# Kernel optimization log

Measured on AMD Instinct MI355X. Metric: run time of the kernel, lower is better.

The kernel has to match this reference:

```python
import jax, jax.numpy as jnp
import numpy as np

B = 8          # batch
HID = 1024     # hidden_size
NH = 8         # query heads
KVH = 1        # kv heads (GQA)
HD = 256       # head_dim
NL = 18        # layers
MLP = 4096     # intermediate size
AH = 50        # action_horizon (suffix len)
AD = 32        # action_dim
P = 1037       # prefix_len
EPS = 1e-6
ROPE_BASE = 10000.0
SCALE = HD ** -0.5
NEG = -2.3819763e38


def _rms(x):
    return x * jax.lax.rsqrt(jnp.mean(x * x, axis=-1, keepdims=True) + EPS)


def _ada_norm(x, cond, W):
    # AdaRMS: cond -> (scale, shift, gate); normed*(1+scale)+shift, gate returned for gated residual
    scale, shift, gate = jnp.split(cond @ W, 3, axis=-1)
    return _rms(x) * (1.0 + scale[:, None, :]) + shift[:, None, :], gate[:, None, :]


def _rope(x, pos):
    # x: [B, heads, S, HD], pos: [B, S]; HF rotate-half convention
    inv = 1.0 / (ROPE_BASE ** (jnp.arange(0, HD, 2, dtype=jnp.float32) / HD))
    freqs = pos[:, :, None].astype(jnp.float32) * inv          # [B,S,HD/2]
    cos = jnp.tile(jnp.cos(freqs), (1, 1, 2))[:, None]          # [B,1,S,HD]
    sin = jnp.tile(jnp.sin(freqs), (1, 1, 2))[:, None]
    x1, x2 = jnp.split(x, 2, axis=-1)
    return x * cos + jnp.concatenate([-x2, x1], axis=-1) * sin


def setup_inputs() -> dict:
    key = jax.random.key(0)
    ks = jax.random.split(key, 24)
    s = 0.02
    return {
        'prefix_keys': jax.random.normal(ks[0], (B, NL, KVH, P, HD), jnp.float32),
        'prefix_values': jax.random.normal(ks[1], (B, NL, KVH, P, HD), jnp.float32),
        'prefix_pad_masks': jnp.ones((B, P), dtype=bool),
        'x_t': jax.random.normal(ks[2], (B, AH, AD), jnp.float32),
        'timestep': jax.random.uniform(ks[3], (B,), jnp.float32),
        'Wq': jax.random.normal(ks[4], (NL, HID, NH * HD), jnp.float32) * s,
        'Wk': jax.random.normal(ks[5], (NL, HID, KVH * HD), jnp.float32) * s,
        'Wv': jax.random.normal(ks[6], (NL, HID, KVH * HD), jnp.float32) * s,
        'Wo': jax.random.normal(ks[7], (NL, NH * HD, HID), jnp.float32) * s,
        'Wg': jax.random.normal(ks[8], (NL, HID, MLP), jnp.float32) * s,
        'Wu': jax.random.normal(ks[9], (NL, HID, MLP), jnp.float32) * s,
        'Wd': jax.random.normal(ks[10], (NL, MLP, HID), jnp.float32) * s,
        'A1': jax.random.normal(ks[11], (NL, HID, 3 * HID), jnp.float32) * s,
        'A2': jax.random.normal(ks[12], (NL, HID, 3 * HID), jnp.float32) * s,
        'Af': jax.random.normal(ks[13], (HID, 3 * HID), jnp.float32) * s,
        'W_act_in': jax.random.normal(ks[14], (AD, HID), jnp.float32) * s,
        'b_act_in': jnp.zeros((HID,), jnp.float32),
        'W_act_out': jax.random.normal(ks[15], (HID, AD), jnp.float32) * s,
        'b_act_out': jnp.zeros((AD,), jnp.float32),
        'W_t_in': jax.random.normal(ks[16], (HID, HID), jnp.float32) * s,
        'b_t_in': jnp.zeros((HID,), jnp.float32),
        'W_t_out': jax.random.normal(ks[17], (HID, HID), jnp.float32) * s,
        'b_t_out': jnp.zeros((HID,), jnp.float32),
    }


def reference(prefix_keys, prefix_values, prefix_pad_masks, x_t, timestep,
              Wq, Wk, Wv, Wo, Wg, Wu, Wd, A1, A2, Af,
              W_act_in, b_act_in, W_act_out, b_act_out,
              W_t_in, b_t_in, W_t_out, b_t_out):
    b = x_t.shape[0]
    # --- time embedding (sinusoidal over log-spaced periods) -> AdaRMS cond ---
    frac = jnp.linspace(0.0, 1.0, HID // 2)
    period = 0.004 * (4.0 / 0.004) ** frac
    sin_in = (2.0 * jnp.pi / period)[None, :] * timestep[:, None]
    temb = jnp.concatenate([jnp.sin(sin_in), jnp.cos(sin_in)], axis=1)  # [B,HID]
    cond = jax.nn.silu(jax.nn.silu(temb @ W_t_in + b_t_in) @ W_t_out + b_t_out)

    # --- action input projection ---
    h = x_t @ W_act_in + b_act_in  # [B,AH,HID]

    # --- attention mask & positions ---
    # suffix att_masks = [1,0,...,0] -> cumsum constant -> suffix block fully visible
    suf_att = jnp.ones((b, AH, AH), dtype=bool)
    s2p = jnp.broadcast_to(prefix_pad_masks[:, None, :], (b, AH, P))
    full = jnp.concatenate([s2p, suf_att], axis=2)          # [B,AH,P+AH]
    bias = jnp.where(full, 0.0, NEG).astype(jnp.float32)[:, None]  # [B,1,AH,P+AH]
    offs = jnp.sum(prefix_pad_masks.astype(jnp.int32), axis=-1, keepdims=True)
    pos = offs + jnp.arange(AH)                              # [B,AH]

    def layer(hcur, p):
        wq, wk, wv, wo, wg, wu, wd, a1, a2, ck, cv = p
        normed, gate = _ada_norm(hcur, cond, a1)
        q = (normed @ wq).reshape(b, AH, NH, HD).transpose(0, 2, 1, 3)
        k = (normed @ wk).reshape(b, AH, KVH, HD).transpose(0, 2, 1, 3)
        v = (normed @ wv).reshape(b, AH, KVH, HD).transpose(0, 2, 1, 3)
        q = _rope(q, pos)
        k = _rope(k, pos)
        fk = jnp.concatenate([ck, k], axis=2)   # [B,KVH,P+AH,HD]
        fv = jnp.concatenate([cv, v], axis=2)
        rep = NH // KVH
        fk = jnp.repeat(fk, rep, axis=1)
        fv = jnp.repeat(fv, rep, axis=1)
        scores = jnp.einsum('bhqd,bhkd->bhqk', q, fk) * SCALE + bias
        attn = jax.nn.softmax(scores, axis=-1)
        o = jnp.einsum('bhqk,bhkd->bhqd', attn, fv)
        o = o.transpose(0, 2, 1, 3).reshape(b, AH, NH * HD) @ wo
        h1 = hcur + gate * o                     # gated residual 1
        n2, gate2 = _ada_norm(h1, cond, a2)
        mlp = (jax.nn.gelu(n2 @ wg, approximate=True) * (n2 @ wu)) @ wd
        return h1 + gate2 * mlp, None            # gated residual 2

    pk = jnp.moveaxis(prefix_keys, 1, 0)   # [NL,B,KVH,P,HD]
    pv = jnp.moveaxis(prefix_values, 1, 0)
    h, _ = jax.lax.scan(layer, h, (Wq, Wk, Wv, Wo, Wg, Wu, Wd, A1, A2, pk, pv))

    out, _ = _ada_norm(h, cond, Af)
    return out @ W_act_out + b_act_out  # [B,AH,AD]
```

## Files before the change

### kernel.cpp

```cpp
#include <hip/hip_runtime.h>

typedef unsigned short u16;
typedef unsigned int   u32;
typedef __attribute__((ext_vector_type(8))) short bh8;
typedef __attribute__((ext_vector_type(4))) float f4;

constexpr int BATCH = 8, HIDN = 1024, NHEAD = 8, HD = 256, NLAY = 18, DMLP = 4096;
constexpr int AHOR = 50, ADIMN = 32, PFXN = 1037, SEQN = 1087, NSTR = 17, MR = 400, MP = 512;
constexpr float EPSV = 1e-6f, NEGV = -2.3819763e38f, QSCALE = 0.0625f;
constexpr size_t ADASL = (size_t)37 * 3 * BATCH * HIDN;
constexpr int SW64 = 90, SW32 = 138, SKT = 266, SPT = 74, SVT = 90;

static __device__ __forceinline__ u16 f2bf(float x){
  union{float f; u32 u;} v; v.f = x;
  u32 r = (v.u + 0x7FFFu + ((v.u >> 16) & 1u)) >> 16;
  return (u16)r;
}
static __device__ __forceinline__ float bf2f(u16 u){
  union{u32 u; float f;} v; v.u = ((u32)u) << 16; return v.f;
}
static __device__ __forceinline__ u32 pack2(float a, float b){
  return (u32)f2bf(a) | ((u32)f2bf(b) << 16);
}
static __device__ __forceinline__ f4 MFMA(bh8 a, bh8 b, f4 c){
  return __builtin_amdgcn_mfma_f32_16x16x32_bf16(a, b, c, 0, 0, 0);
}
static __device__ __forceinline__ float siluf_(float x){ return x / (1.f + __expf(-x)); }
static __device__ __forceinline__ float geluf_(float x){
  float y = 0.7978845608028654f * (x + 0.044715f * x * x * x);
  float e = __expf(2.f * y);
  return 0.5f * x * (2.f - 2.f / (e + 1.f));
}

__global__ void k_prep(const int* __restrict__ mask, const float* __restrict__ ts,
                       float* __restrict__ temb, int* __restrict__ offs,
                       float* __restrict__ ropec, float* __restrict__ ropes)
{
  int t = threadIdx.x;
  {
    int b = t >> 5, l = t & 31;
    const int* mp = mask + b * PFXN;
    int s = 0;
    for (int k = l; k < PFXN; k += 32) s += (mp[k] != 0);
    #pragma unroll
    for (int off = 16; off >= 1; off >>= 1) s += __shfl_xor(s, off);
    if (l == 0) offs[b] = s;
  }
  for (int i = t; i < BATCH * 512; i += 256){
    int b = i >> 9, j = i & 511;
    float frac = (float)j * (1.0f / 511.0f);
    float period = 0.004f * __expf(frac * 6.907755278982137f);
    float arg = (6.283185307179586f / period) * ts[b];
    float s, c; sincosf(arg, &s, &c);
    temb[b * HIDN + j] = s;
    temb[b * HIDN + 512 + j] = c;
  }
  __syncthreads();
  for (int i = t; i < BATCH * AHOR * 128; i += 256){
    int d = i & 127, bt = i >> 7, b = bt / AHOR, tt = bt % AHOR;
    float inv = __expf(-((float)d * (1.f / 128.f)) * 9.210340371976184f);
    float arg = (float)(offs[b] + tt) * inv;
    float s, c; sincosf(arg, &s, &c);
    ropec[i] = c; ropes[i] = s;
  }
}

__global__ void k_tproj(const float* __restrict__ X, const float* __restrict__ W,
                        const float* __restrict__ bias, float* __restrict__ out)
{
  __shared__ float xs[BATCH * HIDN];
  __shared__ float red[BATCH][8][32];
  int t = threadIdx.x;
  for (int i = t; i < BATCH * HIDN; i += 256) xs[i] = X[i];
  __syncthreads();
  int c = t & 31, kp = t >> 5;
  int c0 = blockIdx.x * 32;
  float acc[BATCH];
  #pragma unroll
  for (int b = 0; b < BATCH; ++b) acc[b] = 0.f;
  for (int k = kp * 128; k < kp * 128 + 128; ++k){
    float w = W[(size_t)k * HIDN + c0 + c];
    #pragma unroll
    for (int b = 0; b < BATCH; ++b) acc[b] += xs[b * HIDN + k] * w;
  }
  #pragma unroll
  for (int b = 0; b < BATCH; ++b) red[b][kp][c] = acc[b];
  __syncthreads();
  int b2 = t >> 5, c2 = t & 31;
  float s = bias[c0 + c2];
  #pragma unroll
  for (int kp2 = 0; kp2 < 8; ++kp2) s += red[b2][kp2][c2];
  out[b2 * HIDN + c0 + c2] = siluf_(s);
}

__global__ void k_ada_part(const float* __restrict__ cond, const float* __restrict__ A1,
                           const float* __restrict__ A2, const float* __restrict__ Af,
                           float* __restrict__ adap)
{
  __shared__ float cs[BATCH * 128];
  int t = threadIdx.x;
  int y = blockIdx.y, ks = blockIdx.z;
  int k0 = ks * 128;
  for (int i = t; i < BATCH * 128; i += 256){
    int b = i >> 7, kk = i & 127;
    cs[i] = cond[b * HIDN + k0 + kk];
  }
  __syncthreads();
  const float* A = (y < NLAY) ? (A1 + (size_t)y * HIDN * 3072)
                  : (y < 2 * NLAY) ? (A2 + (size_t)(y - NLAY) * HIDN * 3072) : Af;
  int n = (blockIdx.x * 256 + t) * 4;
  f4 acc[BATCH];
  #pragma unroll
  for (int b = 0; b < BATCH; ++b) acc[b] = (f4){0.f,0.f,0.f,0.f};
  const float* ap = A + (size_t)k0 * 3072 + n;
  for (int kk = 0; kk < 128; kk += 8){
    f4 av[8];
    #pragma unroll
    for (int j = 0; j < 8; ++j) av[j] = *(const f4*)(ap + (size_t)(kk + j) * 3072);
    #pragma unroll
    for (int j = 0; j < 8; ++j){
      #pragma unroll
      for (int b = 0; b < BATCH; ++b) acc[b] += av[j] * cs[b * 128 + kk + j];
    }
  }
  int comp = n >> 10, nn = n & 1023;
  float* o = adap + (size_t)ks * ADASL + ((size_t)y * 3 + comp) * BATCH * HIDN + nn;
  #pragma unroll
  for (int b = 0; b < BATCH; ++b) *(f4*)(o + b * HIDN) = acc[b];
}

__global__ void k_ada_red(const float* __restrict__ adap, float* __restrict__ ada)
{
  size_t i = ((size_t)blockIdx.x * 256 + threadIdx.x) * 8;
  f4 a0 = {0,0,0,0}, a1 = {0,0,0,0};
  #pragma unroll
  for (int ks = 0; ks < 8; ++ks){
    const float* p = adap + (size_t)ks * ADASL + i;
    a0 += *(const f4*)p;
    a1 += *(const f4*)(p + 4);
  }
  *(f4*)(ada + i) = a0;
  *(f4*)(ada + i + 4) = a1;
}

__global__ void k_hin(const float* __restrict__ xt, const float* __restrict__ W,
                      const float* __restrict__ bias, float* __restrict__ h)
{
  int r = blockIdx.x;
  int t = threadIdx.x; int c0 = t * 4;
  __shared__ float xs[ADIMN];
  if (t < ADIMN) xs[t] = xt[r * ADIMN + t];
  __syncthreads();
  float a0 = bias[c0], a1 = bias[c0+1], a2 = bias[c0+2], a3 = bias[c0+3];
  for (int k = 0; k < ADIMN; ++k){
    float x = xs[k];
    const float* wp = W + k * HIDN + c0;
    a0 += x * wp[0]; a1 += x * wp[1]; a2 += x * wp[2]; a3 += x * wp[3];
  }
  float* hp = h + (size_t)r * HIDN + c0;
  hp[0] = a0; hp[1] = a1; hp[2] = a2; hp[3] = a3;
}

__global__ void k_resnorm(int mode, int np,
    const float* __restrict__ base, const u16* __restrict__ parts,
    const float* __restrict__ gate, const float* __restrict__ sc,
    const float* __restrict__ sh, float* __restrict__ outres,
    u16* __restrict__ fragA)
{
  __shared__ float redl[4];
  int t = threadIdx.x;
  int c = t * 4;
  for (int i = 0; i < 2; ++i){
    int r = blockIdx.x * 2 + i;
    bool live = (r < MR);
    float4 v = {0.f,0.f,0.f,0.f};
    int b = live ? (r / AHOR) : 0;
    if (live){
      v = *(const float4*)(base + (size_t)r * HIDN + c);
      if (mode){
        float s0 = 0, s1 = 0, s2 = 0, s3 = 0;
        #pragma unroll 4
        for (int p = 0; p < np; ++p){
          ushort4 u4 = *(const ushort4*)(parts + ((size_t)p * MP + r) * HIDN + c);
          s0 += bf2f(u4.x); s1 += bf2f(u4.y); s2 += bf2f(u4.z); s3 += bf2f(u4.w);
        }
        float4 gp = *(const float4*)(gate + b * HIDN + c);
        v.x += gp.x * s0; v.y += gp.y * s1; v.z += gp.z * s2; v.w += gp.w * s3;
        *(float4*)(outres + (size_t)r * HIDN + c) = v;
      }
    }
    float ss = v.x*v.x + v.y*v.y + v.z*v.z + v.w*v.w;
    #pragma unroll
    for (int off = 1; off < 64; off <<= 1) ss += __shfl_xor(ss, off);
    if ((t & 63) == 0) redl[t >> 6] = ss;
    __syncthreads();
    float tot = redl[0] + redl[1] + redl[2] + redl[3];
    __syncthreads();
    u16* dst = fragA + ((size_t)(c >> 3)) * MP * 8 + (size_t)r * 8 + (c & 7);
    ushort4 ov;
    if (live){
      float rstd = rsqrtf(tot * (1.0f / HIDN) + EPSV);
      const float4 scp = *(const float4*)(sc + b * HIDN + c);
      const float4 shp = *(const float4*)(sh + b * HIDN + c);
      ov.x = f2bf(v.x * rstd * (1.f + scp.x) + shp.x);
      ov.y = f2bf(v.y * rstd * (1.f + scp.y) + shp.y);
      ov.z = f2bf(v.z * rstd * (1.f + scp.z) + shp.z);
      ov.w = f2bf(v.w * rstd * (1.f + scp.w) + shp.w);
    } else {
      ov.x = ov.y = ov.z = ov.w = 0;
    }
    *(ushort4*)dst = ov;
  }
}

template<int NOUTER>
static __device__ __forceinline__ void gemm_core32w(
    const u16* __restrict__ fa,
    const float* __restrict__ Wa, int cb0,
    const float* __restrict__ Wb, int cb1,
    int wN, u16* lds, f4 acc[4][2])
{
  const int tid = threadIdx.x;
  const int lane = tid & 63, wave = tid >> 6;
  const int l15 = lane & 15, g = lane >> 4;
  const int wrow = wave * 64;
  const int c4 = (tid & 7) * 4;
  const int r0 = (tid >> 3) * 2;
  const float* wcol = (c4 < 16) ? (Wa + cb0 + c4) : (Wb + cb1 + (c4 - 16));
  f4 preA[3], preB[3];
  preA[0] = *(const f4*)(wcol + (size_t)r0 * wN);
  preB[0] = *(const f4*)(wcol + (size_t)(r0 + 1) * wN);
  if (NOUTER > 1){
    preA[1] = *(const f4*)(wcol + (size_t)(128 + r0) * wN);
    preB[1] = *(const f4*)(wcol + (size_t)(129 + r0) * wN);
  }
  if (NOUTER > 2){
    preA[2] = *(const f4*)(wcol + (size_t)(256 + r0) * wN);
    preB[2] = *(const f4*)(wcol + (size_t)(257 + r0) * wN);
  }
  #pragma unroll
  for (int i = 0; i < 4; ++i)
    *(u32*)(lds + (c4 + i) * SW32 + r0) = pack2(preA[0][i], preB[0][i]);
  __syncthreads();
  #pragma unroll
  for (int ko = 0; ko < NOUTER; ++ko){
    u16* ldsr = lds + (ko & 1) * (32 * SW32);
    bh8 a01[2][4], a23[2][4];
    #pragma unroll
    for (int kk = 0; kk < 2; ++kk){
      const u16* ap = fa + ((size_t)(ko * 16 + kk * 4 + g) * MP + wrow + l15) * 8;
      #pragma unroll
      for (int mf = 0; mf < 4; ++mf) a01[kk][mf] = *(const bh8*)(ap + mf * 128);
    }
    if (ko + 3 < NOUTER){
      preA[ko % 3] = *(const f4*)(wcol + (size_t)((ko + 3) * 128 + r0) * wN);
      preB[ko % 3] = *(const f4*)(wcol + (size_t)((ko + 3) * 128 + r0 + 1) * wN);
    }
    #pragma unroll
    for (int kk = 2; kk < 4; ++kk){
      const u16* ap = fa + ((size_t)(ko * 16 + kk * 4 + g) * MP + wrow + l15) * 8;
      #pragma unroll
      for (int mf = 0; mf < 4; ++mf) a23[kk - 2][mf] = *(const bh8*)(ap + mf * 128);
    }
    #pragma unroll
    for (int kk = 0; kk < 2; ++kk){
      bh8 bb[2];
      #pragma unroll
      for (int nf = 0; nf < 2; ++nf) bb[nf] = *(const bh8*)(ldsr + (nf * 16 + l15) * SW32 + kk * 32 + g * 8);
      #pragma unroll
      for (int mf = 0; mf < 4; ++mf){
        acc[mf][0] = MFMA(a01[kk][mf], bb[0], acc[mf][0]);
        acc[mf][1] = MFMA(a01[kk][mf], bb[1], acc[mf][1]);
      }
    }
    #pragma unroll
    for (int kk = 2; kk < 4; ++kk){
      bh8 bb[2];
      #pragma unroll
      for (int nf = 0; nf < 2; ++nf) bb[nf] = *(const bh8*)(ldsr + (nf * 16 + l15) * SW32 + kk * 32 + g * 8);
      #pragma unroll
      for (int mf = 0; mf < 4; ++mf){
        acc[mf][0] = MFMA(a23[kk - 2][mf], bb[0], acc[mf][0]);
        acc[mf][1] = MFMA(a23[kk - 2][mf], bb[1], acc[mf][1]);
      }
    }
    if (ko + 1 < NOUTER){
      u16* ldsw = lds + ((ko + 1) & 1) * (32 * SW32);
      const int sl = (ko + 1) % 3;
      #pragma unroll
      for (int i = 0; i < 4; ++i)
        *(u32*)(ldsw + (c4 + i) * SW32 + r0) = pack2(preA[sl][i], preB[sl][i]);
      __syncthreads();
    }
  }
}

__global__ __launch_bounds__(512) void k_qkvrope(
    const u16* __restrict__ n1, const float* __restrict__ Wq,
    const float* __restrict__ Wk, const float* __restrict__ Wv,
    const float* __restrict__ ropec, const float* __restrict__ ropes,
    u16* __restrict__ qf, u16* __restrict__ ks, u16* __restrict__ vs)
{
  __shared__ u16 lds[2 * 32 * SW32];
  int bx = blockIdx.x;
  const float *Wa, *Wb; int cb0, cb1, wN, type, head = 0, fb = 0, d0 = 0;
  if (bx < 64){ type = 0; head = bx >> 3; fb = (bx & 7) * 16; Wa = Wq; Wb = Wq; wN = NHEAD * HD; cb0 = head * HD + fb; cb1 = cb0 + 128; }
  else if (bx < 72){ type = 1; fb = (bx - 64) * 16; Wa = Wk; Wb = Wk; wN = HD; cb0 = fb; cb1 = fb + 128; }
  else { type = 2; d0 = (bx - 72) * 32; Wa = Wv; Wb = Wv; wN = HD; cb0 = d0; cb1 = d0 + 16; }
  f4 acc[4][2];
  #pragma unroll
  for (int i = 0; i < 4; ++i)
    #pragma unroll
    for (int j = 0; j < 2; ++j) acc[i][j] = (f4){0.f, 0.f, 0.f, 0.f};
  gemm_core32w<8>(n1, Wa, cb0, Wb, cb1, wN, lds, acc);
  int tid = threadIdx.x, lane = tid & 63, wave = tid >> 6, l15 = lane & 15, g = lane >> 4;
  int wrow = wave * 64;
  #pragma unroll
  for (int mf = 0; mf < 4; ++mf)
    #pragma unroll
    for (int r = 0; r < 4; ++r){
      int row = wrow + mf * 16 + 4 * g + r;
      if (row >= MR) continue;
      int b = row / AHOR, tt = row - b * AHOR;
      float lo = acc[mf][0][r], hi = acc[mf][1][r];
      if (type == 2){
        size_t vb = ((size_t)(b * AHOR + tt)) * HD;
        vs[vb + d0 + l15] = f2bf(lo);
        vs[vb + d0 + 16 + l15] = f2bf(hi);
      } else {
        int dA = fb + l15;
        float cz = ropec[(size_t)(b * AHOR + tt) * 128 + dA];
        float sz = ropes[(size_t)(b * AHOR + tt) * 128 + dA];
        float oA = lo * cz - hi * sz;
        float oB = hi * cz + lo * sz;
        if (type == 0){
          oA *= QSCALE; oB *= QSCALE;
          int rowp = head * AHOR + tt;
          int dB = dA + 128;
          qf[((size_t)(b * 32 + (dA >> 3))) * MP * 8 + (size_t)rowp * 8 + (dA & 7)] = f2bf(oA);
          qf[((size_t)(b * 32 + (dB >> 3))) * MP * 8 + (size_t)rowp * 8 + (dB & 7)] = f2bf(oB);
        } else {
          size_t kb = ((size_t)(b * AHOR + tt)) * HD;
          ks[kb + dA] = f2bf(oA);
          ks[kb + dA + 128] = f2bf(oB);
        }
      }
    }
}

__global__ __launch_bounds__(512) void k_attn(
    const u16* __restrict__ qf, const u16* __restrict__ kss, const u16* __restrict__ vss,
    const float* __restrict__ pk, const float* __restrict__ pv,
    const int* __restrict__ mask, int layer,
    u16* __restrict__ opart, float* __restrict__ mrow, float* __restrict__ lrow)
{
  __shared__ u16 kv[256 * SVT];
  __shared__ u16 plds[256 * SPT];
  int s = blockIdx.x, b = blockIdx.y, z = blockIdx.z;
  int tid = threadIdx.x, lane = tid & 63, wave = tid >> 6, l15 = lane & 15, g = lane >> 4;
  int zb = z * 256;
  int wbase = wave * 32;
  {
    int key = tid >> 3, dblk = (tid & 7) * 32;
    int kg = s * 64 + key;
    u32* dst = (u32*)(kv + key * SKT + dblk);
    if (kg < PFXN){
      const float4* src = (const float4*)(pk + (((size_t)b * NLAY + layer) * PFXN + kg) * HD + dblk);
      #pragma unroll
      for (int j = 0; j < 8; ++j){ float4 v = src[j]; dst[2*j] = pack2(v.x, v.y); dst[2*j+1] = pack2(v.z, v.w); }
    } else if (kg < SEQN){
      const u32* src = (const u32*)(kss + ((size_t)b * AHOR + (kg - PFXN)) * HD + dblk);
      #pragma unroll
      for (int j = 0; j < 16; ++j) dst[j] = src[j];
    } else {
      #pragma unroll
      for (int j = 0; j < 16; ++j) dst[j] = 0;
    }
  }
  float vreg[32];
  int vkey = tid >> 3, vdb = (tid & 7) * 32;
  {
    int kgv = s * 64 + vkey;
    if (kgv < PFXN){
      const float4* src = (const float4*)(pv + (((size_t)b * NLAY + layer) * PFXN + kgv) * HD + vdb);
      #pragma unroll
      for (int j = 0; j < 8; ++j){ float4 v = src[j]; vreg[4*j] = v.x; vreg[4*j+1] = v.y; vreg[4*j+2] = v.z; vreg[4*j+3] = v.w; }
    } else if (kgv < SEQN){
      const u32* src = (const u32*)(vss + ((size_t)b * AHOR + (kgv - PFXN)) * HD + vdb);
      #pragma unroll
      for (int j = 0; j < 16; ++j){ u32 u = src[j]; vreg[2*j] = bf2f((u16)(u & 0xFFFF)); vreg[2*j+1] = bf2f((u16)(u >> 16)); }
    } else {
      #pragma unroll
      for (int j = 0; j < 32; ++j) vreg[j] = 0.f;
    }
  }
  bool valid[4];
  #pragma unroll
  for (int nf = 0; nf < 4; ++nf){
    int kgc = s * 64 + nf * 16 + l15;
    valid[nf] = (kgc < PFXN) ? (mask[b * PFXN + kgc] != 0) : (kgc < SEQN);
  }
  __syncthreads();
  f4 acc[2][4];
  #pragma unroll
  for (int i = 0; i < 2; ++i)
    #pragma unroll
    for (int j = 0; j < 4; ++j) acc[i][j] = (f4){0.f,0.f,0.f,0.f};
  const u16* qb = qf + (size_t)b * 32 * MP * 8;
  #pragma unroll
  for (int ko = 0; ko < 4; ++ko)
    #pragma unroll
    for (int kk = 0; kk < 2; ++kk){
      int kc = ko * 8 + kk * 4 + g;
      bh8 a[2], bb[4];
      const u16* ap = qb + ((size_t)kc * MP + zb + wbase + l15) * 8;
      #pragma unroll
      for (int mf = 0; mf < 2; ++mf) a[mf] = *(const bh8*)(ap + mf * 128);
      #pragma unroll
      for (int nf = 0; nf < 4; ++nf) bb[nf] = *(const bh8*)(kv + (nf * 16 + l15) * SKT + ko * 64 + kk * 32 + g * 8);
      #pragma unroll
      for (int mf = 0; mf < 2; ++mf)
        #pragma unroll
        for (int nf = 0; nf < 4; ++nf) acc[mf][nf] = MFMA(a[mf], bb[nf], acc[mf][nf]);
    }
  #pragma unroll
  for (int nf = 0; nf < 4; ++nf) if (!valid[nf]){
    #pragma unroll
    for (int mf = 0; mf < 2; ++mf){
      acc[mf][nf][0] = NEGV; acc[mf][nf][1] = NEGV; acc[mf][nf][2] = NEGV; acc[mf][nf][3] = NEGV;
    }
  }
  #pragma unroll
  for (int mf = 0; mf < 2; ++mf)
    #pragma unroll
    for (int r = 0; r < 4; ++r){
      float m0 = fmaxf(fmaxf(acc[mf][0][r], acc[mf][1][r]), fmaxf(acc[mf][2][r], acc[mf][3][r]));
      #pragma unroll
      for (int off = 1; off < 16; off <<= 1) m0 = fmaxf(m0, __shfl_xor(m0, off));
      int lr = wbase + mf * 16 + 4 * g + r;
      float sum = 0.f;
      #pragma unroll
      for (int nf = 0; nf < 4; ++nf){
        float p = __expf(acc[mf][nf][r] - m0);
        sum += p;
        plds[lr * SPT + nf * 16 + l15] = f2bf(p);
      }
      #pragma unroll
      for (int off = 1; off < 16; off <<= 1) sum += __shfl_xor(sum, off);
      if (l15 == 0){
        mrow[((size_t)b * NSTR + s) * MP + zb + lr] = m0;
        lrow[((size_t)b * NSTR + s) * MP + zb + lr] = sum;
      }
    }
  __syncthreads();
  {
    #pragma unroll
    for (int j = 0; j < 32; ++j){
      int dloc = vdb + j;
      kv[dloc * SVT + ((dloc >> 5) & 3) * 8 + vkey] = f2bf(vreg[j]);
    }
  }
  __syncthreads();
  #pragma unroll
  for (int dc = 0; dc < 4; ++dc){
    f4 oc[2][4];
    #pragma unroll
    for (int i = 0; i < 2; ++i)
      #pragma unroll
      for (int j = 0; j < 4; ++j) oc[i][j] = (f4){0.f,0.f,0.f,0.f};
    #pragma unroll
    for (int kk = 0; kk < 2; ++kk){
      bh8 a[2], bb[4];
      #pragma unroll
      for (int mf = 0; mf < 2; ++mf) a[mf] = *(const bh8*)(plds + (wbase + mf * 16 + l15) * SPT + kk * 32 + g * 8);
      #pragma unroll
      for (int nf = 0; nf < 4; ++nf){
        int dcol = dc * 64 + nf * 16 + l15;
        bb[nf] = *(const bh8*)(kv + dcol * SVT + ((dcol >> 5) & 3) * 8 + kk * 32 + g * 8);
      }
      #pragma unroll
      for (int mf = 0; mf < 2; ++mf)
        #pragma unroll
        for (int nf = 0; nf < 4; ++nf) oc[mf][nf] = MFMA(a[mf], bb[nf], oc[mf][nf]);
    }
    #pragma unroll
    for (int mf = 0; mf < 2; ++mf)
      #pragma unroll
      for (int r = 0; r < 4; ++r){
        int row = zb + wbase + mf * 16 + 4 * g + r;
        if (row < MR){
          #pragma unroll
          for (int nf = 0; nf < 4; ++nf){
            int d = dc * 64 + nf * 16 + l15;
            opart[(((size_t)b * NSTR + s) * MR + row) * HD + d] = f2bf(oc[mf][nf][r]);
          }
        }
      }
  }
}

__global__ void k_comb(const u16* __restrict__ opart, const float* __restrict__ mrow,
                       const float* __restrict__ lrow, u16* __restrict__ ao)
{
  int b = blockIdx.y;
  int t = threadIdx.x;
  int d4 = (t & 63) * 4;
  int row = blockIdx.x * 4 + (t >> 6);
  float M = -3.0e38f;
  for (int s2 = 0; s2 < NSTR; ++s2) M = fmaxf(M, mrow[((size_t)b * NSTR + s2) * MP + row]);
  float L = 0.f;
  float o0 = 0.f, o1 = 0.f, o2 = 0.f, o3 = 0.f;
  for (int s2 = 0; s2 < NSTR; ++s2){
    float w = __expf(mrow[((size_t)b * NSTR + s2) * MP + row] - M);
    L += w * lrow[((size_t)b * NSTR + s2) * MP + row];
    ushort4 u4 = *(const ushort4*)(opart + (((size_t)b * NSTR + s2) * MR + row) * HD + d4);
    o0 += w * bf2f(u4.x); o1 += w * bf2f(u4.y); o2 += w * bf2f(u4.z); o3 += w * bf2f(u4.w);
  }
  float rL = 1.0f / L;
  int h = row / AHOR, tt = row - h * AHOR;
  int col = h * HD + d4;
  int rg = b * AHOR + tt;
  ushort4 ov;
  ov.x = f2bf(o0 * rL); ov.y = f2bf(o1 * rL); ov.z = f2bf(o2 * rL); ov.w = f2bf(o3 * rL);
  *(ushort4*)(ao + ((size_t)(col >> 3)) * MP * 8 + (size_t)rg * 8 + (col & 7)) = ov;
}

template<int NOUTER>
__global__ __launch_bounds__(512) void k_gemm_part32(
    const u16* __restrict__ fa, const float* __restrict__ W, int wN,
    u16* __restrict__ outp)
{
  __shared__ u16 lds[2 * 32 * SW32];
  int n0 = blockIdx.x * 32;
  int ksl = blockIdx.y;
  const u16* fa_s = fa + (size_t)(ksl * NOUTER * 16) * MP * 8;
  const float* W_s = W + (size_t)(ksl * NOUTER * 128) * wN;
  f4 acc[4][2];
  #pragma unroll
  for (int i = 0; i < 4; ++i)
    #pragma unroll
    for (int j = 0; j < 2; ++j) acc[i][j] = (f4){0.f,0.f,0.f,0.f};
  gemm_core32w<NOUTER>(fa_s, W_s, n0, W_s, n0 + 16, wN, lds, acc);
  int tid = threadIdx.x, lane = tid & 63, wave = tid >> 6, l15 = lane & 15, g = lane >> 4;
  int wrow = wave * 64;
  #pragma unroll
  for (int mf = 0; mf < 4; ++mf)
    #pragma unroll
    for (int r = 0; r < 4; ++r){
      int row = wrow + mf * 16 + 4 * g + r;
      outp[((size_t)ksl * MP + row) * 1024 + n0 + l15] = f2bf(acc[mf][0][r]);
      outp[((size_t)ksl * MP + row) * 1024 + n0 + 16 + l15] = f2bf(acc[mf][1][r]);
    }
}

__global__ __launch_bounds__(512) void k_mlpup(
    const u16* __restrict__ n2, const float* __restrict__ Wg, const float* __restrict__ Wu,
    u16* __restrict__ mlpf)
{
  __shared__ u16 lds[2 * 32 * SW32];
  int n0 = blockIdx.x * 16;
  f4 acc[4][2];
  #pragma unroll
  for (int i = 0; i < 4; ++i)
    #pragma unroll
    for (int j = 0; j < 2; ++j) acc[i][j] = (f4){0.f,0.f,0.f,0.f};
  gemm_core32w<8>(n2, Wg, n0, Wu, n0, DMLP, lds, acc);
  int tid = threadIdx.x, lane = tid & 63, wave = tid >> 6, l15 = lane & 15, g = lane >> 4;
  int wrow = wave * 64;
  #pragma unroll
  for (int mf = 0; mf < 4; ++mf)
    #pragma unroll
    for (int r = 0; r < 4; ++r){
      int row = wrow + mf * 16 + 4 * g + r;
      int col = n0 + l15;
      float gg = acc[mf][0][r], uu = acc[mf][1][r];
      float act = geluf_(gg) * uu;
      mlpf[((size_t)(col >> 3)) * MP * 8 + (size_t)row * 8 + (col & 7)] = f2bf(act);
    }
}

__global__ void k_out(const u16* __restrict__ nfr, const float* __restrict__ W,
                      const float* __restrict__ bias, float* __restrict__ out)
{
  int t = threadIdx.x;
  int row = blockIdx.x * 8 + (t >> 5);
  int c = t & 31;
  float acc = bias[c];
  for (int kc = 0; kc < 128; ++kc){
    bh8 v = *(const bh8*)(nfr + ((size_t)kc * MP + row) * 8);
    #pragma unroll
    for (int j = 0; j < 8; ++j)
      acc += bf2f((u16)v[j]) * W[(kc * 8 + j) * ADIMN + c];
  }
  out[row * ADIMN + c] = acc;
}

extern "C" void kernel_launch(void* const* d_in, const int* in_sizes, int n_in,
                              void* d_out, int out_size, void* d_ws, size_t ws_size,
                              hipStream_t stream)
{
  const float* pk  = (const float*)d_in[0];
  const float* pv  = (const float*)d_in[1];
  const int*   msk = (const int*)d_in[2];
  const float* xt  = (const float*)d_in[3];
  const float* ts  = (const float*)d_in[4];
  const float* Wq  = (const float*)d_in[5];
  const float* Wk  = (const float*)d_in[6];
  const float* Wv  = (const float*)d_in[7];
  const float* Wo  = (const float*)d_in[8];
  const float* Wg  = (const float*)d_in[9];
  const float* Wu  = (const float*)d_in[10];
  const float* Wd  = (const float*)d_in[11];
  const float* A1  = (const float*)d_in[12];
  const float* A2  = (const float*)d_in[13];
  const float* Af  = (const float*)d_in[14];
  const float* Wai = (const float*)d_in[15];
  const float* bai = (const float*)d_in[16];
  const float* Wao = (const float*)d_in[17];
  const float* bao = (const float*)d_in[18];
  const float* Wti = (const float*)d_in[19];
  const float* bti = (const float*)d_in[20];
  const float* Wto = (const float*)d_in[21];
  const float* bto = (const float*)d_in[22];

  char* w = (char*)d_ws;
  size_t off = 0;
  auto alloc = [&](size_t bytes) -> char* {
    char* p = w + off; off += (bytes + 255) & ~(size_t)255; return p;
  };
  float* temb  = (float*)alloc((size_t)BATCH * HIDN * 4);
  float* ttmp  = (float*)alloc((size_t)BATCH * HIDN * 4);
  float* cond  = (float*)alloc((size_t)BATCH * HIDN * 4);
  int*   offs  = (int*)alloc(BATCH * 4);
  float* ropec = (float*)alloc((size_t)BATCH * AHOR * 128 * 4);
  float* ropes = (float*)alloc((size_t)BATCH * AHOR * 128 * 4);
  float* ada   = (float*)alloc(ADASL * 4);
  float* adap  = (float*)alloc(8 * ADASL * 4);
  float* h     = (float*)alloc((size_t)MR * HIDN * 4);
  float* h1    = (float*)alloc((size_t)MR * HIDN * 4);
  u16*   n1    = (u16*)alloc((size_t)128 * MP * 8 * 2);
  u16*   n2    = (u16*)alloc((size_t)128 * MP * 8 * 2);
  u16*   qf    = (u16*)alloc((size_t)BATCH * 32 * MP * 8 * 2);
  u16*   kss   = (u16*)alloc((size_t)BATCH * AHOR * HD * 2);
  u16*   vss   = (u16*)alloc((size_t)BATCH * AHOR * HD * 2);
  u16*   opart = (u16*)alloc((size_t)BATCH * NSTR * MR * HD * 2);
  float* mrow  = (float*)alloc((size_t)BATCH * NSTR * MP * 4);
  float* lrow  = (float*)alloc((size_t)BATCH * NSTR * MP * 4);
  u16*   ao    = (u16*)alloc((size_t)256 * MP * 8 * 2);
  u16*   opp   = (u16*)alloc((size_t)8 * MP * 1024 * 2);
  u16*   mlpf  = (u16*)alloc((size_t)512 * MP * 8 * 2);
  u16*   mdp   = (u16*)alloc((size_t)8 * MP * 1024 * 2);
  if (off > ws_size) return;

  k_prep<<<1, 256, 0, stream>>>(msk, ts, temb, offs, ropec, ropes);
  k_tproj<<<32, 256, 0, stream>>>(temb, Wti, bti, ttmp);
  k_tproj<<<32, 256, 0, stream>>>(ttmp, Wto, bto, cond);
  k_ada_part<<<dim3(3, 37, 8), 256, 0, stream>>>(cond, A1, A2, Af, adap);
  k_ada_red<<<444, 256, 0, stream>>>(adap, ada);
  k_hin<<<MR, 256, 0, stream>>>(xt, Wai, bai, h);

  auto AP = [&](int y, int comp){ return ada + ((size_t)y * 3 + comp) * BATCH * HIDN; };

  k_resnorm<<<256, 256, 0, stream>>>(0, 0, h, nullptr, nullptr, AP(0,0), AP(0,1), nullptr, n1);

  for (int l = 0; l < NLAY; ++l){
    k_qkvrope<<<80, 512, 0, stream>>>(n1, Wq + (size_t)l * HIDN * NHEAD * HD,
                                      Wk + (size_t)l * HIDN * HD, Wv + (size_t)l * HIDN * HD,
                                      ropec, ropes, qf, kss, vss);
    k_attn<<<dim3(NSTR, BATCH, 2), 512, 0, stream>>>(qf, kss, vss, pk, pv, msk, l, opart, mrow, lrow);
    k_comb<<<dim3(100, BATCH), 256, 0, stream>>>(opart, mrow, lrow, ao);
    k_gemm_part32<2><<<dim3(32, 8), 512, 0, stream>>>(ao, Wo + (size_t)l * 2048 * 1024, 1024, opp);
    k_resnorm<<<256, 256, 0, stream>>>(1, 8, h, opp, AP(l,2), AP(NLAY+l,0), AP(NLAY+l,1), h1, n2);
    k_mlpup<<<256, 512, 0, stream>>>(n2, Wg + (size_t)l * HIDN * DMLP, Wu + (size_t)l * HIDN * DMLP, mlpf);
    k_gemm_part32<4><<<dim3(32, 8), 512, 0, stream>>>(mlpf, Wd + (size_t)l * DMLP * 1024, 1024, mdp);
    const float* nsc = (l < NLAY - 1) ? AP(l + 1, 0) : AP(36, 0);
    const float* nsh = (l < NLAY - 1) ? AP(l + 1, 1) : AP(36, 1);
    k_resnorm<<<256, 256, 0, stream>>>(2, 8, h1, mdp, AP(NLAY+l,2), nsc, nsh, h, n1);
  }
  k_out<<<50, 256, 0, stream>>>(n1, Wao, bao, (float*)d_out);
}
```

Measured before the change: 2.832 ms.

## Process two key tiles per attention block with online softmax, halving split count

```diff
diff --git a/kernel.cpp b/kernel.cpp
--- a/kernel.cpp
+++ b/kernel.cpp
@@ -6,10 +6,11 @@
 typedef __attribute__((ext_vector_type(4))) float f4;
 
 constexpr int BATCH = 8, HIDN = 1024, NHEAD = 8, HD = 256, NLAY = 18, DMLP = 4096;
-constexpr int AHOR = 50, ADIMN = 32, PFXN = 1037, SEQN = 1087, NSTR = 17, MR = 400, MP = 512;
+constexpr int AHOR = 50, ADIMN = 32, PFXN = 1037, SEQN = 1087, MR = 400, MP = 512;
+constexpr int NGRP = 9;
 constexpr float EPSV = 1e-6f, NEGV = -2.3819763e38f, QSCALE = 0.0625f;
 constexpr size_t ADASL = (size_t)37 * 3 * BATCH * HIDN;
-constexpr int SW64 = 90, SW32 = 138, SKT = 266, SPT = 74, SVT = 90;
+constexpr int SW32 = 138, SKT = 266, SPT = 74, SVT = 90;
 
 static __device__ __forceinline__ u16 f2bf(float x){
   union{float f; u32 u;} v; v.f = x;
@@ -360,129 +361,159 @@
   int tid = threadIdx.x, lane = tid & 63, wave = tid >> 6, l15 = lane & 15, g = lane >> 4;
   int zb = z * 256;
   int wbase = wave * 32;
-  {
-    int key = tid >> 3, dblk = (tid & 7) * 32;
-    int kg = s * 64 + key;
-    u32* dst = (u32*)(kv + key * SKT + dblk);
-    if (kg < PFXN){
-      const float4* src = (const float4*)(pk + (((size_t)b * NLAY + layer) * PFXN + kg) * HD + dblk);
-      #pragma unroll
-      for (int j = 0; j < 8; ++j){ float4 v = src[j]; dst[2*j] = pack2(v.x, v.y); dst[2*j+1] = pack2(v.z, v.w); }
-    } else if (kg < SEQN){
-      const u32* src = (const u32*)(kss + ((size_t)b * AHOR + (kg - PFXN)) * HD + dblk);
-      #pragma unroll
-      for (int j = 0; j < 16; ++j) dst[j] = src[j];
-    } else {
-      #pragma unroll
-      for (int j = 0; j < 16; ++j) dst[j] = 0;
-    }
-  }
-  float vreg[32];
-  int vkey = tid >> 3, vdb = (tid & 7) * 32;
-  {
-    int kgv = s * 64 + vkey;
-    if (kgv < PFXN){
-      const float4* src = (const float4*)(pv + (((size_t)b * NLAY + layer) * PFXN + kgv) * HD + vdb);
-      #pragma unroll
-      for (int j = 0; j < 8; ++j){ float4 v = src[j]; vreg[4*j] = v.x; vreg[4*j+1] = v.y; vreg[4*j+2] = v.z; vreg[4*j+3] = v.w; }
-    } else if (kgv < SEQN){
-      const u32* src = (const u32*)(vss + ((size_t)b * AHOR + (kgv - PFXN)) * HD + vdb);
-      #pragma unroll
-      for (int j = 0; j < 16; ++j){ u32 u = src[j]; vreg[2*j] = bf2f((u16)(u & 0xFFFF)); vreg[2*j+1] = bf2f((u16)(u >> 16)); }
-    } else {
-      #pragma unroll
-      for (int j = 0; j < 32; ++j) vreg[j] = 0.f;
-    }
-  }
-  bool valid[4];
-  #pragma unroll
-  for (int nf = 0; nf < 4; ++nf){
-    int kgc = s * 64 + nf * 16 + l15;
-    valid[nf] = (kgc < PFXN) ? (mask[b * PFXN + kgc] != 0) : (kgc < SEQN);
-  }
-  __syncthreads();
-  f4 acc[2][4];
-  #pragma unroll
-  for (int i = 0; i < 2; ++i)
-    #pragma unroll
-    for (int j = 0; j < 4; ++j) acc[i][j] = (f4){0.f,0.f,0.f,0.f};
-  const u16* qb = qf + (size_t)b * 32 * MP * 8;
-  #pragma unroll
-  for (int ko = 0; ko < 4; ++ko)
-    #pragma unroll
-    for (int kk = 0; kk < 2; ++kk){
-      int kc = ko * 8 + kk * 4 + g;
-      bh8 a[2], bb[4];
-      const u16* ap = qb + ((size_t)kc * MP + zb + wbase + l15) * 8;
-      #pragma unroll
-      for (int mf = 0; mf < 2; ++mf) a[mf] = *(const bh8*)(ap + mf * 128);
-      #pragma unroll
-      for (int nf = 0; nf < 4; ++nf) bb[nf] = *(const bh8*)(kv + (nf * 16 + l15) * SKT + ko * 64 + kk * 32 + g * 8);
-      #pragma unroll
-      for (int mf = 0; mf < 2; ++mf)
-        #pragma unroll
-        for (int nf = 0; nf < 4; ++nf) acc[mf][nf] = MFMA(a[mf], bb[nf], acc[mf][nf]);
-    }
-  #pragma unroll
-  for (int nf = 0; nf < 4; ++nf) if (!valid[nf]){
-    #pragma unroll
-    for (int mf = 0; mf < 2; ++mf){
-      acc[mf][nf][0] = NEGV; acc[mf][nf][1] = NEGV; acc[mf][nf][2] = NEGV; acc[mf][nf][3] = NEGV;
-    }
-  }
+  f4 oc[4][2][4];
+  #pragma unroll
+  for (int dc = 0; dc < 4; ++dc)
+    #pragma unroll
+    for (int mf = 0; mf < 2; ++mf)
+      #pragma unroll
+      for (int nf = 0; nf < 4; ++nf) oc[dc][mf][nf] = (f4){0.f,0.f,0.f,0.f};
+  float mrun[2][4], lrun[2][4];
   #pragma unroll
   for (int mf = 0; mf < 2; ++mf)
     #pragma unroll
+    for (int r = 0; r < 4; ++r){ mrun[mf][r] = -3.0e38f; lrun[mf][r] = 0.f; }
+
+  #pragma unroll
+  for (int kt = 0; kt < 2; ++kt){
+    int kbase = s * 128 + kt * 64;
+    {
+      int key = tid >> 3, dblk = (tid & 7) * 32;
+      int kg = kbase + key;
+      u32* dst = (u32*)(kv + key * SKT + dblk);
+      if (kg < PFXN){
+        const float4* src = (const float4*)(pk + (((size_t)b * NLAY + layer) * PFXN + kg) * HD + dblk);
+        #pragma unroll
+        for (int j = 0; j < 8; ++j){ float4 v = src[j]; dst[2*j] = pack2(v.x, v.y); dst[2*j+1] = pack2(v.z, v.w); }
+      } else if (kg < SEQN){
+        const u32* src = (const u32*)(kss + ((size_t)b * AHOR + (kg - PFXN)) * HD + dblk);
+        #pragma unroll
+        for (int j = 0; j < 16; ++j) dst[j] = src[j];
+      } else {
+        #pragma unroll
+        for (int j = 0; j < 16; ++j) dst[j] = 0;
+      }
+    }
+    float vreg[32];
+    int vkey = tid >> 3, vdb = (tid & 7) * 32;
+    {
+      int kgv = kbase + vkey;
+      if (kgv < PFXN){
+        const float4* src = (const float4*)(pv + (((size_t)b * NLAY + layer) * PFXN + kgv) * HD + vdb);
+        #pragma unroll
+        for (int j = 0; j < 8; ++j){ float4 v = src[j]; vreg[4*j] = v.x; vreg[4*j+1] = v.y; vreg[4*j+2] = v.z; vreg[4*j+3] = v.w; }
+      } else if (kgv < SEQN){
+        const u32* src = (const u32*)(vss + ((size_t)b * AHOR + (kgv - PFXN)) * HD + vdb);
+        #pragma unroll
+        for (int j = 0; j < 16; ++j){ u32 u = src[j]; vreg[2*j] = bf2f((u16)(u & 0xFFFF)); vreg[2*j+1] = bf2f((u16)(u >> 16)); }
+      } else {
+        #pragma unroll
+        for (int j = 0; j < 32; ++j) vreg[j] = 0.f;
+      }
+    }
+    bool valid[4];
+    #pragma unroll
+    for (int nf = 0; nf < 4; ++nf){
+      int kgc = kbase + nf * 16 + l15;
+      valid[nf] = (kgc < PFXN) ? (mask[b * PFXN + kgc] != 0) : (kgc < SEQN);
+    }
+    __syncthreads();
+    f4 acc[2][4];
+    #pragma unroll
+    for (int i = 0; i < 2; ++i)
+      #pragma unroll
+      for (int j = 0; j < 4; ++j) acc[i][j] = (f4){0.f,0.f,0.f,0.f};
+    const u16* qb = qf + (size_t)b * 32 * MP * 8;
+    #pragma unroll
+    for (int ko = 0; ko < 4; ++ko)
+      #pragma unroll
+      for (int kk = 0; kk < 2; ++kk){
+        int kc = ko * 8 + kk * 4 + g;
+        bh8 a[2], bb[4];
+        const u16* ap = qb + ((size_t)kc * MP + zb + wbase + l15) * 8;
+        #pragma unroll
+        for (int mf = 0; mf < 2; ++mf) a[mf] = *(const bh8*)(ap + mf * 128);
+        #pragma unroll
+        for (int nf = 0; nf < 4; ++nf) bb[nf] = *(const bh8*)(kv + (nf * 16 + l15) * SKT + ko * 64 + kk * 32 + g * 8);
+        #pragma unroll
+        for (int mf = 0; mf < 2; ++mf)
+          #pragma unroll
+          for (int nf = 0; nf < 4; ++nf) acc[mf][nf] = MFMA(a[mf], bb[nf], acc[mf][nf]);
+      }
+    #pragma unroll
+    for (int nf = 0; nf < 4; ++nf) if (!valid[nf]){
+      #pragma unroll
+      for (int mf = 0; mf < 2; ++mf){
+        acc[mf][nf][0] = NEGV; acc[mf][nf][1] = NEGV; acc[mf][nf][2] = NEGV; acc[mf][nf][3] = NEGV;
+      }
+    }
+    #pragma unroll
+    for (int mf = 0; mf < 2; ++mf)
+      #pragma unroll
+      for (int r = 0; r < 4; ++r){
+        float mt = fmaxf(fmaxf(acc[mf][0][r], acc[mf][1][r]), fmaxf(acc[mf][2][r], acc[mf][3][r]));
+        #pragma unroll
+        for (int off = 1; off < 16; off <<= 1) mt = fmaxf(mt, __shfl_xor(mt, off));
+        float mnew = fmaxf(mrun[mf][r], mt);
+        float alpha = __expf(mrun[mf][r] - mnew);
+        int lr = wbase + mf * 16 + 4 * g + r;
+        float sum = 0.f;
+        #pragma unroll
+        for (int nf = 0; nf < 4; ++nf){
+          float p = __expf(acc[mf][nf][r] - mnew);
+          sum += p;
+          plds[lr * SPT + nf * 16 + l15] = f2bf(p);
+        }
+        #pragma unroll
+        for (int off = 1; off < 16; off <<= 1) sum += __shfl_xor(sum, off);
+        lrun[mf][r] = alpha * lrun[mf][r] + sum;
+        mrun[mf][r] = mnew;
+        #pragma unroll
+        for (int dc = 0; dc < 4; ++dc)
+          #pragma unroll
+          for (int nf = 0; nf < 4; ++nf) oc[dc][mf][nf][r] *= alpha;
+      }
+    __syncthreads();
+    {
+      #pragma unroll
+      for (int j = 0; j < 32; ++j){
+        int dloc = vdb + j;
+        kv[dloc * SVT + ((dloc >> 5) & 3) * 8 + vkey] = f2bf(vreg[j]);
+      }
+    }
+    __syncthreads();
+    #pragma unroll
+    for (int dc = 0; dc < 4; ++dc){
+      #pragma unroll
+      for (int kk = 0; kk < 2; ++kk){
+        bh8 a[2], bb[4];
+        #pragma unroll
+        for (int mf = 0; mf < 2; ++mf) a[mf] = *(const bh8*)(plds + (wbase + mf * 16 + l15) * SPT + kk * 32 + g * 8);
+        #pragma unroll
+        for (int nf = 0; nf < 4; ++nf){
+          int dcol = dc * 64 + nf * 16 + l15;
+          bb[nf] = *(const bh8*)(kv + dcol * SVT + ((dcol >> 5) & 3) * 8 + kk * 32 + g * 8);
+        }
+        #pragma unroll
+        for (int mf = 0; mf < 2; ++mf)
+          #pragma unroll
+          for (int nf = 0; nf < 4; ++nf) oc[dc][mf][nf] = MFMA(a[mf], bb[nf], oc[dc][mf][nf]);
+      }
+    }
+    __syncthreads();
+  }
+  #pragma unroll
+  for (int mf = 0; mf < 2; ++mf)
+    #pragma unroll
     for (int r = 0; r < 4; ++r){
-      float m0 = fmaxf(fmaxf(acc[mf][0][r], acc[mf][1][r]), fmaxf(acc[mf][2][r], acc[mf][3][r]));
-      #pragma unroll
-      for (int off = 1; off < 16; off <<= 1) m0 = fmaxf(m0, __shfl_xor(m0, off));
       int lr = wbase + mf * 16 + 4 * g + r;
-      float sum = 0.f;
-      #pragma unroll
-      for (int nf = 0; nf < 4; ++nf){
-        float p = __expf(acc[mf][nf][r] - m0);
-        sum += p;
-        plds[lr * SPT + nf * 16 + l15] = f2bf(p);
-      }
-      #pragma unroll
-      for (int off = 1; off < 16; off <<= 1) sum += __shfl_xor(sum, off);
       if (l15 == 0){
-        mrow[((size_t)b * NSTR + s) * MP + zb + lr] = m0;
-        lrow[((size_t)b * NSTR + s) * MP + zb + lr] = sum;
-      }
-    }
-  __syncthreads();
-  {
-    #pragma unroll
-    for (int j = 0; j < 32; ++j){
-      int dloc = vdb + j;
-      kv[dloc * SVT + ((dloc >> 5) & 3) * 8 + vkey] = f2bf(vreg[j]);
-    }
-  }
-  __syncthreads();
-  #pragma unroll
-  for (int dc = 0; dc < 4; ++dc){
-    f4 oc[2][4];
-    #pragma unroll
-    for (int i = 0; i < 2; ++i)
-      #pragma unroll
-      for (int j = 0; j < 4; ++j) oc[i][j] = (f4){0.f,0.f,0.f,0.f};
-    #pragma unroll
-    for (int kk = 0; kk < 2; ++kk){
-      bh8 a[2], bb[4];
-      #pragma unroll
-      for (int mf = 0; mf < 2; ++mf) a[mf] = *(const bh8*)(plds + (wbase + mf * 16 + l15) * SPT + kk * 32 + g * 8);
-      #pragma unroll
-      for (int nf = 0; nf < 4; ++nf){
-        int dcol = dc * 64 + nf * 16 + l15;
-        bb[nf] = *(const bh8*)(kv + dcol * SVT + ((dcol >> 5) & 3) * 8 + kk * 32 + g * 8);
-      }
-      #pragma unroll
-      for (int mf = 0; mf < 2; ++mf)
-        #pragma unroll
-        for (int nf = 0; nf < 4; ++nf) oc[mf][nf] = MFMA(a[mf], bb[nf], oc[mf][nf]);
-    }
+        mrow[((size_t)b * NGRP + s) * MP + zb + lr] = mrun[mf][r];
+        lrow[((size_t)b * NGRP + s) * MP + zb + lr] = lrun[mf][r];
+      }
+    }
+  #pragma unroll
+  for (int dc = 0; dc < 4; ++dc)
     #pragma unroll
     for (int mf = 0; mf < 2; ++mf)
       #pragma unroll
@@ -492,11 +523,10 @@
           #pragma unroll
           for (int nf = 0; nf < 4; ++nf){
             int d = dc * 64 + nf * 16 + l15;
-            opart[(((size_t)b * NSTR + s) * MR + row) * HD + d] = f2bf(oc[mf][nf][r]);
+            opart[(((size_t)b * NGRP + s) * MR + row) * HD + d] = f2bf(oc[dc][mf][nf][r]);
           }
         }
       }
-  }
 }
 
 __global__ void k_comb(const u16* __restrict__ opart, const float* __restrict__ mrow,
@@ -507,13 +537,13 @@
   int d4 = (t & 63) * 4;
   int row = blockIdx.x * 4 + (t >> 6);
   float M = -3.0e38f;
-  for (int s2 = 0; s2 < NSTR; ++s2) M = fmaxf(M, mrow[((size_t)b * NSTR + s2) * MP + row]);
+  for (int s2 = 0; s2 < NGRP; ++s2) M = fmaxf(M, mrow[((size_t)b * NGRP + s2) * MP + row]);
   float L = 0.f;
   float o0 = 0.f, o1 = 0.f, o2 = 0.f, o3 = 0.f;
-  for (int s2 = 0; s2 < NSTR; ++s2){
-    float w = __expf(mrow[((size_t)b * NSTR + s2) * MP + row] - M);
-    L += w * lrow[((size_t)b * NSTR + s2) * MP + row];
-    ushort4 u4 = *(const ushort4*)(opart + (((size_t)b * NSTR + s2) * MR + row) * HD + d4);
+  for (int s2 = 0; s2 < NGRP; ++s2){
+    float w = __expf(mrow[((size_t)b * NGRP + s2) * MP + row] - M);
+    L += w * lrow[((size_t)b * NGRP + s2) * MP + row];
+    ushort4 u4 = *(const ushort4*)(opart + (((size_t)b * NGRP + s2) * MR + row) * HD + d4);
     o0 += w * bf2f(u4.x); o1 += w * bf2f(u4.y); o2 += w * bf2f(u4.z); o3 += w * bf2f(u4.w);
   }
   float rL = 1.0f / L;
@@ -643,9 +673,9 @@
   u16*   qf    = (u16*)alloc((size_t)BATCH * 32 * MP * 8 * 2);
   u16*   kss   = (u16*)alloc((size_t)BATCH * AHOR * HD * 2);
   u16*   vss   = (u16*)alloc((size_t)BATCH * AHOR * HD * 2);
-  u16*   opart = (u16*)alloc((size_t)BATCH * NSTR * MR * HD * 2);
-  float* mrow  = (float*)alloc((size_t)BATCH * NSTR * MP * 4);
-  float* lrow  = (float*)alloc((size_t)BATCH * NSTR * MP * 4);
+  u16*   opart = (u16*)alloc((size_t)BATCH * NGRP * MR * HD * 2);
+  float* mrow  = (float*)alloc((size_t)BATCH * NGRP * MP * 4);
+  float* lrow  = (float*)alloc((size_t)BATCH * NGRP * MP * 4);
   u16*   ao    = (u16*)alloc((size_t)256 * MP * 8 * 2);
   u16*   opp   = (u16*)alloc((size_t)8 * MP * 1024 * 2);
   u16*   mlpf  = (u16*)alloc((size_t)512 * MP * 8 * 2);
@@ -667,7 +697,7 @@
     k_qkvrope<<<80, 512, 0, stream>>>(n1, Wq + (size_t)l * HIDN * NHEAD * HD,
                                       Wk + (size_t)l * HIDN * HD, Wv + (size_t)l * HIDN * HD,
                                       ropec, ropes, qf, kss, vss);
-    k_attn<<<dim3(NSTR, BATCH, 2), 512, 0, stream>>>(qf, kss, vss, pk, pv, msk, l, opart, mrow, lrow);
+    k_attn<<<dim3(NGRP, BATCH, 2), 512, 0, stream>>>(qf, kss, vss, pk, pv, msk, l, opart, mrow, lrow);
     k_comb<<<dim3(100, BATCH), 256, 0, stream>>>(opart, mrow, lrow, ao);
     k_gemm_part32<2><<<dim3(32, 8), 512, 0, stream>>>(ao, Wo + (size_t)l * 2048 * 1024, 1024, opp);
     k_resnorm<<<256, 256, 0, stream>>>(1, 8, h, opp, AP(l,2), AP(NLAY+l,0), AP(NLAY+l,1), h1, n2);
```

After: 2.833 ms. Within noise of the previous version (+0.0%).
